# Performance work log

Hardware: AMD Instinct MI355X
Metric: run time of the kernel (lower is better)

Reference implementation:

```python
import jax, jax.numpy as jnp
import numpy as np

S, B, C = 7, 2, 1
LAMBDA_COORD, LAMBDA_NOOBJ = 5.0, 0.5
EPS = 1e-6
BATCH = 32768


def setup_inputs() -> dict:
    key = jax.random.key(0)
    k1, k2, k3, k4 = jax.random.split(key, 4)
    predictions = jax.random.normal(k1, (BATCH, S, S, B * 5 + C), dtype=jnp.float32)
    coords = jax.random.uniform(k2, (BATCH, S, S, 4), dtype=jnp.float32) * 0.9 + 0.05
    conf = jax.random.randint(k3, (BATCH, S, S, 1), 0, 2).astype(jnp.float32)  # exactly 0 or 1
    cls = jax.random.randint(k4, (BATCH, S, S, C), 0, 2).astype(jnp.float32)
    targets = jnp.concatenate([coords, conf, cls], axis=-1)  # [BATCH,S,S,6]
    return {"predictions": predictions, "targets": targets}


def reference(predictions, targets):
    dt = predictions.dtype
    obj = (targets[..., 4] == 1.0).astype(dt)      # [bs,S,S]
    noobj = (targets[..., 4] == 0.0).astype(dt)    # [bs,S,S]

    pb = predictions[..., : B * 5].reshape(predictions.shape[:-1] + (B, 5))  # [bs,S,S,B,5]
    tb = targets[..., :5]                                                    # [bs,S,S,5]

    # IoU of each of the B predicted boxes vs the target box (per cell)
    sxy = jax.nn.sigmoid(pb[..., 0:2])
    awh = jnp.abs(pb[..., 2:4])
    p1 = sxy - awh / 2
    p2 = sxy + awh / 2
    t1 = tb[..., 0:2] - tb[..., 2:4] / 2
    t2 = tb[..., 0:2] + tb[..., 2:4] / 2
    lo = jnp.maximum(p1, t1[..., None, :])
    hi = jnp.minimum(p2, t2[..., None, :])
    inter = jnp.prod(jnp.maximum(hi - lo, 0.0), axis=-1)        # [bs,S,S,B]
    parea = jnp.prod(jnp.abs(p2 - p1), axis=-1)                 # [bs,S,S,B]
    tarea = (tb[..., 2] * tb[..., 3])[..., None]
    iou = inter / (parea + tarea - inter + EPS)

    best = jnp.argmax(iou, axis=-1)                             # [bs,S,S]
    bb = jnp.take_along_axis(pb, best[..., None, None], axis=-2)[..., 0, :]  # [bs,S,S,5]

    coord = LAMBDA_COORD * jnp.sum(
        obj * jnp.sum((jax.nn.sigmoid(bb[..., 0:2]) - tb[..., 0:2]) ** 2, axis=-1)
    )
    coord = coord + LAMBDA_COORD * jnp.sum(
        obj * jnp.sum((jnp.sqrt(jnp.abs(bb[..., 2:4]) + EPS) - jnp.sqrt(tb[..., 2:4] + EPS)) ** 2, axis=-1)
    )

    conf_obj = jnp.sum(obj * (jax.nn.sigmoid(bb[..., 4]) - tb[..., 4]) ** 2)

    conf_noobj = LAMBDA_NOOBJ * jnp.sum(
        noobj[..., None] * (jax.nn.sigmoid(pb[..., 4]) - tb[..., 4:5]) ** 2
    )

    # C == 1: binary cross-entropy with logits, summed over obj cells
    pc = predictions[..., B * 5 : B * 5 + C]
    tc = targets[..., 5 : 5 + C]
    bce = jnp.maximum(pc, 0.0) - pc * tc + jnp.log1p(jnp.exp(-jnp.abs(pc)))
    class_loss = jnp.sum(obj[..., None] * bce)

    bs = predictions.shape[0]
    total = (coord + conf_obj + conf_noobj + class_loss) / bs
    return (total, coord / bs, conf_obj / bs, conf_noobj / bs, class_loss / bs)
```

## Files before the change

kernel.cpp:

```cpp
#include <hip/hip_runtime.h>
#include <math.h>


#define PRED_C 11
#define TGT_C  6
#define CPB    256
#define LAMBDA_COORD 5.0f
#define LAMBDA_NOOBJ 0.5f
#define EPSV 1e-6f

__device__ __forceinline__ float fsig(float x) {
    return __builtin_amdgcn_rcpf(1.0f + __expf(-x));
}

__global__ __launch_bounds__(CPB) void yolo_partial_kernel(
    const float* __restrict__ pred,
    const float* __restrict__ tgt,
    float* __restrict__ partials)
{
    __shared__ float sp[CPB * PRED_C];
    __shared__ float st[CPB * TGT_C];
    __shared__ float red[4][4];

    const int tid = threadIdx.x;
    const long long blockCell = (long long)blockIdx.x * CPB;

    {
        const float4* gp = (const float4*)(pred + blockCell * PRED_C);
        float4* lp = (float4*)sp;
        lp[tid] = gp[tid];
        lp[tid + 256] = gp[tid + 256];
        if (tid < CPB * PRED_C / 4 - 512) lp[tid + 512] = gp[tid + 512];
        const float4* gt = (const float4*)(tgt + blockCell * TGT_C);
        float4* lt = (float4*)st;
        lt[tid] = gt[tid];
        if (tid < CPB * TGT_C / 4 - 256) lt[tid + 256] = gt[tid + 256];
    }
    __syncthreads();

    const float* p = sp + tid * PRED_C;
    const float* t = st + tid * TGT_C;

    const float tx = t[0], ty = t[1], tw = t[2], th = t[3];
    const float tconf = t[4], tcls = t[5];
    const float obj   = (tconf == 1.0f) ? 1.0f : 0.0f;
    const float noobj = (tconf == 0.0f) ? 1.0f : 0.0f;

    const float t1x = tx - tw * 0.5f, t1y = ty - th * 0.5f;
    const float t2x = tx + tw * 0.5f, t2y = ty + th * 0.5f;
    const float tarea = tw * th;

    float iou[2], sx[2], sy[2], aw[2], ah[2], scf[2];
    #pragma unroll
    for (int b = 0; b < 2; ++b) {
        const float px = p[b * 5 + 0], py = p[b * 5 + 1];
        const float pw = p[b * 5 + 2], ph = p[b * 5 + 3];
        sx[b] = fsig(px);
        sy[b] = fsig(py);
        scf[b] = fsig(p[b * 5 + 4]);
        aw[b] = fabsf(pw);
        ah[b] = fabsf(ph);
        const float p1x = sx[b] - aw[b] * 0.5f, p1y = sy[b] - ah[b] * 0.5f;
        const float p2x = sx[b] + aw[b] * 0.5f, p2y = sy[b] + ah[b] * 0.5f;
        const float ix = fminf(p2x, t2x) - fmaxf(p1x, t1x);
        const float iy = fminf(p2y, t2y) - fmaxf(p1y, t1y);
        const float inter = fmaxf(ix, 0.0f) * fmaxf(iy, 0.0f);
        const float parea = aw[b] * ah[b];
        iou[b] = inter * __builtin_amdgcn_rcpf(parea + tarea - inter + EPSV);
    }
    const int best = (iou[1] > iou[0]) ? 1 : 0;

    const float dx = sx[best] - tx;
    const float dy = sy[best] - ty;
    const float dw = __builtin_amdgcn_sqrtf(aw[best] + EPSV) -
                     __builtin_amdgcn_sqrtf(tw + EPSV);
    const float dh = __builtin_amdgcn_sqrtf(ah[best] + EPSV) -
                     __builtin_amdgcn_sqrtf(th + EPSV);
    float coord = LAMBDA_COORD * obj * ((dx * dx + dy * dy) + (dw * dw + dh * dh));

    const float sc = scf[best];
    float conf_obj = obj * (sc - tconf) * (sc - tconf);

    const float d0 = scf[0] - tconf;
    const float d1 = scf[1] - tconf;
    float conf_noobj = LAMBDA_NOOBJ * noobj * (d0 * d0 + d1 * d1);

    const float pc = p[10];
    const float bce = fmaxf(pc, 0.0f) - pc * tcls + __logf(1.0f + __expf(-fabsf(pc)));
    float class_loss = obj * bce;

    #pragma unroll
    for (int off = 32; off >= 1; off >>= 1) {
        coord      += __shfl_down(coord, off);
        conf_obj   += __shfl_down(conf_obj, off);
        conf_noobj += __shfl_down(conf_noobj, off);
        class_loss += __shfl_down(class_loss, off);
    }
    const int wave = tid >> 6;
    const int lane = tid & 63;
    if (lane == 0) {
        red[wave][0] = coord;
        red[wave][1] = conf_obj;
        red[wave][2] = conf_noobj;
        red[wave][3] = class_loss;
    }
    __syncthreads();
    if (tid == 0) {
        float4 v;
        v.x = red[0][0] + red[1][0] + red[2][0] + red[3][0];
        v.y = red[0][1] + red[1][1] + red[2][1] + red[3][1];
        v.z = red[0][2] + red[1][2] + red[2][2] + red[3][2];
        v.w = red[0][3] + red[1][3] + red[2][3] + red[3][3];
        ((float4*)partials)[blockIdx.x] = v;
    }
}

__global__ __launch_bounds__(1024) void yolo_final_kernel(
    const float* __restrict__ partials,
    float* __restrict__ out,
    int nblk,
    float inv_bs)
{
    __shared__ float red[16][4];
    const int tid = threadIdx.x;

    float c = 0.f, co = 0.f, cn = 0.f, cl = 0.f;
    for (int i = tid; i < nblk; i += 1024) {
        const float4 v = ((const float4*)partials)[i];
        c += v.x; co += v.y; cn += v.z; cl += v.w;
    }
    #pragma unroll
    for (int off = 32; off >= 1; off >>= 1) {
        c  += __shfl_down(c, off);
        co += __shfl_down(co, off);
        cn += __shfl_down(cn, off);
        cl += __shfl_down(cl, off);
    }
    const int wave = tid >> 6;
    const int lane = tid & 63;
    if (lane == 0) {
        red[wave][0] = c;
        red[wave][1] = co;
        red[wave][2] = cn;
        red[wave][3] = cl;
    }
    __syncthreads();
    if (tid == 0) {
        float sc = 0.f, sco = 0.f, scn = 0.f, scl = 0.f;
        #pragma unroll
        for (int w = 0; w < 16; ++w) {
            sc  += red[w][0];
            sco += red[w][1];
            scn += red[w][2];
            scl += red[w][3];
        }
        out[0] = (sc + sco + scn + scl) * inv_bs;
        out[1] = sc  * inv_bs;
        out[2] = sco * inv_bs;
        out[3] = scn * inv_bs;
        out[4] = scl * inv_bs;
    }
}

extern "C" void kernel_launch(void* const* d_in, const int* in_sizes, int n_in,
                              void* d_out, int out_size, void* d_ws, size_t ws_size,
                              hipStream_t stream) {
    const float* pred = (const float*)d_in[0];
    const float* tgt  = (const float*)d_in[1];
    float* out = (float*)d_out;
    float* partials = (float*)d_ws;

    const long long batch = (long long)in_sizes[0] / (7 * 7 * PRED_C);
    const long long cells = batch * 49;
    const int nblk = (int)(cells / CPB);

    yolo_partial_kernel<<<nblk, CPB, 0, stream>>>(pred, tgt, partials);
    yolo_final_kernel<<<1, 1024, 0, stream>>>(partials, out, nblk,
                                              1.0f / (float)batch);
}
```

Measured before the change: 132.3 us.

## Load cells directly from global with unaligned vectors, two cells per thread

Drops the LDS staging buffers and the block barrier. Each thread now loads its own cells straight from global memory with unaligned 4-wide and 2-wide vector loads, using overlapping reads for the 11-float prediction record. Each thread processes two cells, which halves the block count and the reduction overhead. In exchange the per-thread strided loads are less coalesced (44-byte and 24-byte strides across lanes) and the overlapping loads re-read one float per cell. Whether the caches absorb this is uncertain.

```diff
diff --git a/kernel.cpp b/kernel.cpp
--- a/kernel.cpp
+++ b/kernel.cpp
@@ -4,45 +4,25 @@
 
 #define PRED_C 11
 #define TGT_C  6
-#define CPB    256
+#define TPB    256
+#define CELLS_PER_THREAD 2
 #define LAMBDA_COORD 5.0f
 #define LAMBDA_NOOBJ 0.5f
 #define EPSV 1e-6f
+
+typedef float f4u __attribute__((ext_vector_type(4), aligned(4)));
+typedef float f2u __attribute__((ext_vector_type(2), aligned(4)));
 
 __device__ __forceinline__ float fsig(float x) {
     return __builtin_amdgcn_rcpf(1.0f + __expf(-x));
 }
 
-__global__ __launch_bounds__(CPB) void yolo_partial_kernel(
-    const float* __restrict__ pred,
-    const float* __restrict__ tgt,
-    float* __restrict__ partials)
+__device__ __forceinline__ void cell_loss(f4u a, f4u b, f4u c, f4u t4, f2u t2,
+                                          float& acc_coord, float& acc_cobj,
+                                          float& acc_cnoobj, float& acc_cls)
 {
-    __shared__ float sp[CPB * PRED_C];
-    __shared__ float st[CPB * TGT_C];
-    __shared__ float red[4][4];
-
-    const int tid = threadIdx.x;
-    const long long blockCell = (long long)blockIdx.x * CPB;
-
-    {
-        const float4* gp = (const float4*)(pred + blockCell * PRED_C);
-        float4* lp = (float4*)sp;
-        lp[tid] = gp[tid];
-        lp[tid + 256] = gp[tid + 256];
-        if (tid < CPB * PRED_C / 4 - 512) lp[tid + 512] = gp[tid + 512];
-        const float4* gt = (const float4*)(tgt + blockCell * TGT_C);
-        float4* lt = (float4*)st;
-        lt[tid] = gt[tid];
-        if (tid < CPB * TGT_C / 4 - 256) lt[tid + 256] = gt[tid + 256];
-    }
-    __syncthreads();
-
-    const float* p = sp + tid * PRED_C;
-    const float* t = st + tid * TGT_C;
-
-    const float tx = t[0], ty = t[1], tw = t[2], th = t[3];
-    const float tconf = t[4], tcls = t[5];
+    const float tx = t4.x, ty = t4.y, tw = t4.z, th = t4.w;
+    const float tconf = t2.x, tcls = t2.y;
     const float obj   = (tconf == 1.0f) ? 1.0f : 0.0f;
     const float noobj = (tconf == 0.0f) ? 1.0f : 0.0f;
 
@@ -50,23 +30,27 @@
     const float t2x = tx + tw * 0.5f, t2y = ty + th * 0.5f;
     const float tarea = tw * th;
 
+    const float px[2] = { a.x, b.y };
+    const float py[2] = { a.y, b.z };
+    const float pw[2] = { a.z, b.w };
+    const float ph[2] = { a.w, c.y };
+    const float pf[2] = { b.x, c.z };
+
     float iou[2], sx[2], sy[2], aw[2], ah[2], scf[2];
     #pragma unroll
-    for (int b = 0; b < 2; ++b) {
-        const float px = p[b * 5 + 0], py = p[b * 5 + 1];
-        const float pw = p[b * 5 + 2], ph = p[b * 5 + 3];
-        sx[b] = fsig(px);
-        sy[b] = fsig(py);
-        scf[b] = fsig(p[b * 5 + 4]);
-        aw[b] = fabsf(pw);
-        ah[b] = fabsf(ph);
-        const float p1x = sx[b] - aw[b] * 0.5f, p1y = sy[b] - ah[b] * 0.5f;
-        const float p2x = sx[b] + aw[b] * 0.5f, p2y = sy[b] + ah[b] * 0.5f;
+    for (int bb = 0; bb < 2; ++bb) {
+        sx[bb]  = fsig(px[bb]);
+        sy[bb]  = fsig(py[bb]);
+        scf[bb] = fsig(pf[bb]);
+        aw[bb]  = fabsf(pw[bb]);
+        ah[bb]  = fabsf(ph[bb]);
+        const float p1x = sx[bb] - aw[bb] * 0.5f, p1y = sy[bb] - ah[bb] * 0.5f;
+        const float p2x = sx[bb] + aw[bb] * 0.5f, p2y = sy[bb] + ah[bb] * 0.5f;
         const float ix = fminf(p2x, t2x) - fmaxf(p1x, t1x);
         const float iy = fminf(p2y, t2y) - fmaxf(p1y, t1y);
         const float inter = fmaxf(ix, 0.0f) * fmaxf(iy, 0.0f);
-        const float parea = aw[b] * ah[b];
-        iou[b] = inter * __builtin_amdgcn_rcpf(parea + tarea - inter + EPSV);
+        const float parea = aw[bb] * ah[bb];
+        iou[bb] = inter * __builtin_amdgcn_rcpf(parea + tarea - inter + EPSV);
     }
     const int best = (iou[1] > iou[0]) ? 1 : 0;
 
@@ -76,33 +60,65 @@
                      __builtin_amdgcn_sqrtf(tw + EPSV);
     const float dh = __builtin_amdgcn_sqrtf(ah[best] + EPSV) -
                      __builtin_amdgcn_sqrtf(th + EPSV);
-    float coord = LAMBDA_COORD * obj * ((dx * dx + dy * dy) + (dw * dw + dh * dh));
+    acc_coord += LAMBDA_COORD * obj * ((dx * dx + dy * dy) + (dw * dw + dh * dh));
 
     const float sc = scf[best];
-    float conf_obj = obj * (sc - tconf) * (sc - tconf);
+    acc_cobj += obj * (sc - tconf) * (sc - tconf);
 
     const float d0 = scf[0] - tconf;
     const float d1 = scf[1] - tconf;
-    float conf_noobj = LAMBDA_NOOBJ * noobj * (d0 * d0 + d1 * d1);
+    acc_cnoobj += LAMBDA_NOOBJ * noobj * (d0 * d0 + d1 * d1);
 
-    const float pc = p[10];
-    const float bce = fmaxf(pc, 0.0f) - pc * tcls + __logf(1.0f + __expf(-fabsf(pc)));
-    float class_loss = obj * bce;
+    const float pc = c.w;
+    const float bce = fmaxf(pc, 0.0f) - pc * tcls +
+                      __logf(1.0f + __expf(-fabsf(pc)));
+    acc_cls += obj * bce;
+}
+
+__global__ __launch_bounds__(TPB) void yolo_partial_kernel(
+    const float* __restrict__ pred,
+    const float* __restrict__ tgt,
+    float* __restrict__ partials)
+{
+    __shared__ float red[4][4];
+    const int tid = threadIdx.x;
+    const long long c0 = (long long)blockIdx.x * (TPB * CELLS_PER_THREAD) + tid;
+    const long long c1 = c0 + TPB;
+
+    const float* p0 = pred + c0 * PRED_C;
+    const float* p1 = pred + c1 * PRED_C;
+    const float* t0 = tgt  + c0 * TGT_C;
+    const float* t1 = tgt  + c1 * TGT_C;
+
+    const f4u a0 = *(const f4u*)(p0);
+    const f4u b0 = *(const f4u*)(p0 + 4);
+    const f4u cc0 = *(const f4u*)(p0 + 7);
+    const f4u a1 = *(const f4u*)(p1);
+    const f4u b1 = *(const f4u*)(p1 + 4);
+    const f4u cc1 = *(const f4u*)(p1 + 7);
+    const f4u t40 = *(const f4u*)(t0);
+    const f2u t20 = *(const f2u*)(t0 + 4);
+    const f4u t41 = *(const f4u*)(t1);
+    const f2u t21 = *(const f2u*)(t1 + 4);
+
+    float coord = 0.f, cobj = 0.f, cnoobj = 0.f, cls = 0.f;
+    cell_loss(a0, b0, cc0, t40, t20, coord, cobj, cnoobj, cls);
+    cell_loss(a1, b1, cc1, t41, t21, coord, cobj, cnoobj, cls);
 
     #pragma unroll
     for (int off = 32; off >= 1; off >>= 1) {
-        coord      += __shfl_down(coord, off);
-        conf_obj   += __shfl_down(conf_obj, off);
-        conf_noobj += __shfl_down(conf_noobj, off);
-        class_loss += __shfl_down(class_loss, off);
+        coord  += __shfl_down(coord, off);
+        cobj   += __shfl_down(cobj, off);
+        cnoobj += __shfl_down(cnoobj, off);
+        cls    += __shfl_down(cls, off);
     }
     const int wave = tid >> 6;
     const int lane = tid & 63;
     if (lane == 0) {
         red[wave][0] = coord;
-        red[wave][1] = conf_obj;
-        red[wave][2] = conf_noobj;
-        red[wave][3] = class_loss;
+        red[wave][1] = cobj;
+        red[wave][2] = cnoobj;
+        red[wave][3] = cls;
     }
     __syncthreads();
     if (tid == 0) {
@@ -172,9 +188,9 @@
 
     const long long batch = (long long)in_sizes[0] / (7 * 7 * PRED_C);
     const long long cells = batch * 49;
-    const int nblk = (int)(cells / CPB);
+    const int nblk = (int)(cells / (TPB * CELLS_PER_THREAD));
 
-    yolo_partial_kernel<<<nblk, CPB, 0, stream>>>(pred, tgt, partials);
+    yolo_partial_kernel<<<nblk, TPB, 0, stream>>>(pred, tgt, partials);
     yolo_final_kernel<<<1, 1024, 0, stream>>>(partials, out, nblk,
                                               1.0f / (float)batch);
 }
```

New measurement: 129.8 us. No clear change (-1.9%).
